# Kernel optimization log

Hardware: AMD Instinct MI355X
Metric: run time of the kernel (lower is better)

## Reference

```python
import jax, jax.numpy as jnp
import numpy as np

L, N, C = 8192, 8, 3
DIM, DIM_OUT, K, RATIO = 64, 128, 16, 0.25
L2 = int(L * RATIO)  # 2048; note L % L2 == 0 (needed for the fmod quirk)
EPS = 1e-5


def layer_norm(x, g, b):
    m = jnp.mean(x, axis=-1, keepdims=True)
    v = jnp.mean(jnp.square(x - m), axis=-1, keepdims=True)  # biased var, as torch LayerNorm
    return (x - m) * jax.lax.rsqrt(v + EPS) * g + b


def mlp(x, w1, g1, b1, w2, g2, b2):
    h = x @ w1.T
    h = layer_norm(h, g1, b1)
    h = h @ w2.T
    h = layer_norm(h, g2, b2)
    return jax.nn.relu(h)


def setup_inputs() -> dict:
    key = jax.random.key(0)
    ks = jax.random.split(key, 5)
    coords = jax.random.normal(ks[0], (L, N, C), jnp.float32)
    features = jax.random.normal(ks[1], (L, N, DIM), jnp.float32)
    s1 = 1.0 / np.sqrt(DIM)
    s2 = 1.0 / np.sqrt(DIM_OUT)
    w1 = jax.random.uniform(ks[2], (DIM_OUT, DIM), jnp.float32, -s1, s1)
    w2 = jax.random.uniform(ks[3], (DIM_OUT, DIM_OUT), jnp.float32, -s2, s2)
    g1 = jnp.ones((DIM_OUT,), jnp.float32)
    b1 = jnp.zeros((DIM_OUT,), jnp.float32)
    g2 = jnp.ones((DIM_OUT,), jnp.float32)
    b2 = jnp.zeros((DIM_OUT,), jnp.float32)
    # RandomDecimate: random permutation of point indices, keep first L2 (same across batch)
    keep_idx = jax.random.permutation(ks[4], L)[:L2].astype(jnp.int32)
    return dict(coords=coords, features=features, w1=w1, g1=g1, b1=b1,
                w2=w2, g2=g2, b2=b2, keep_idx=keep_idx)


def reference(coords, features, w1, g1, b1, w2, g2, b2, keep_idx):
    # MLP on all points: [L, N, DIM_OUT]
    feats = mlp(features, w1, g1, b1, w2, g2, b2)
    # decimation: keep_coords [L2, N, C]
    keep_coords = coords[keep_idx]
    # per-batch KNN of kept points against all points
    c = coords.transpose(1, 0, 2)        # [N, L, C]
    kc = keep_coords.transpose(1, 0, 2)  # [N, L2, C]
    d2 = (jnp.sum(kc * kc, -1)[:, :, None]
          + jnp.sum(c * c, -1)[:, None, :]
          - 2.0 * jnp.einsum('nic,njc->nij', kc, c))  # [N, L2, L]
    _, nn_idx = jax.lax.top_k(-d2, K)    # [N, L2, K] indices into [0, L)
    # faithful to clusters.fmod_(L2) on flattened idx n*L+l (L % L2 == 0 => l % L2)
    nn_idx = nn_idx % L2
    # fused gather + amax pooling over K neighbors
    fT = feats.transpose(1, 0, 2)  # [N, L, DIM_OUT]
    gathered = jax.vmap(lambda f, idx: f[idx])(fT, nn_idx)  # [N, L2, K, DIM_OUT]
    pool_features = jnp.max(gathered, axis=2).transpose(1, 0, 2)  # [L2, N, DIM_OUT]
    return keep_coords, pool_features
```

## Files before the change

### kernel.cpp

```cpp
#include <hip/hip_runtime.h>
#include <stdint.h>

#define L_    8192
#define N_    8
#define L2_   2048
#define K_    16

typedef unsigned int uint;
typedef unsigned short ushort;
typedef unsigned long long u64;
typedef __attribute__((ext_vector_type(8))) short bh8;
typedef __attribute__((ext_vector_type(4))) float f32x4;

__device__ __forceinline__ ushort f2b(float f){
  uint u = __float_as_uint(f);
  return (ushort)((u + 0x7FFFu + ((u >> 16) & 1u)) >> 16);
}
__device__ __forceinline__ uint ford(float f){
  uint u = __float_as_uint(f);
  return u ^ ((uint)((int)u >> 31) | 0x80000000u);
}
__device__ __forceinline__ float unford(uint u){
  uint v = (u & 0x80000000u) ? (u ^ 0x80000000u) : ~u;
  return __uint_as_float(v);
}

__device__ __forceinline__ void ld8(float* t, const float* p){
  float4 a = *(const float4*)p; float4 b = *(const float4*)(p + 4);
  t[0]=a.x; t[1]=a.y; t[2]=a.z; t[3]=a.w; t[4]=b.x; t[5]=b.y; t[6]=b.z; t[7]=b.w;
}
__device__ __forceinline__ bh8 pack8(const float* v){
  bh8 r;
  #pragma unroll
  for (int j = 0; j < 8; ++j) r[j] = (short)f2b(v[j]);
  return r;
}

__global__ __launch_bounds__(256) void prep_pack_k(const float* __restrict__ coords,
                                                   const int* __restrict__ keep,
                                                   const float* __restrict__ w1,
                                                   const float* __restrict__ w2,
                                                   float4* __restrict__ cF,
                                                   float* __restrict__ out0,
                                                   ushort* __restrict__ pw1,
                                                   ushort* __restrict__ pw2){
  int blk = blockIdx.x;
  int tid = threadIdx.x;
  if (blk < 96){
    int e = blk * 256 + tid;
    if (e < 8192) pw1[e] = f2b(w1[e]);
    else          pw2[e - 8192] = f2b(w2[e - 8192]);
  } else if (blk < 352){
    int e = (blk - 96) * 256 + tid;
    int l = e >> 3, n = e & 7;
    const float* cr = coords + (size_t)e * 3;
    float x = cr[0], y = cr[1], z = cr[2];
    float cc;
    {
      #pragma clang fp contract(off)
      cc = x*x + y*y + z*z;
    }
    cF[n * L_ + l] = make_float4(x, y, z, cc);
  } else {
    int t = (blk - 352) * 256 + tid;
    int i = t / 24; int rem = t - i * 24;
    out0[t] = coords[(size_t)keep[i] * 24 + rem];
  }
}

__global__ __launch_bounds__(256) void mlp_k(const float* __restrict__ feat,
                                             const ushort* __restrict__ pw1,
                                             const float* __restrict__ g1,
                                             const float* __restrict__ b1,
                                             const ushort* __restrict__ pw2,
                                             const float* __restrict__ g2,
                                             const float* __restrict__ b2,
                                             uint* __restrict__ fBw){
  __shared__ ushort hlds[64 * 136];
  int tid = threadIdx.x;
  int lane = tid & 63;
  int wv = __builtin_amdgcn_readfirstlane(tid >> 6);
  int quad = lane >> 4, c = lane & 15;
  int rowg = blockIdx.x * 64 + wv * 16;

  bh8 a1[2];
  {
    int rg = rowg + c; int l = rg & 2047, nb = rg >> 11;
    const float* xr = feat + (size_t)((l << 3) + nb) * 64 + quad * 8;
    float t[8];
    ld8(t, xr);      a1[0] = pack8(t);
    ld8(t, xr + 32); a1[1] = pack8(t);
  }

  f32x4 acc1[8];
  #pragma unroll
  for (int t = 0; t < 8; ++t) acc1[t] = (f32x4){0.f, 0.f, 0.f, 0.f};
  #pragma unroll
  for (int s = 0; s < 2; ++s){
    #pragma unroll
    for (int t = 0; t < 8; ++t){
      bh8 wb = *(const bh8*)(pw1 + (size_t)(t * 16 + c) * 64 + s * 32 + quad * 8);
      acc1[t] = __builtin_amdgcn_mfma_f32_16x16x32_bf16(a1[s], wb, acc1[t], 0, 0, 0);
    }
  }

  float mean1[4], rstd1[4];
  #pragma unroll
  for (int r = 0; r < 4; ++r){
    float s = 0.f;
    #pragma unroll
    for (int t = 0; t < 8; ++t) s += acc1[t][r];
    #pragma unroll
    for (int m = 1; m < 16; m <<= 1) s += __shfl_xor(s, m, 16);
    mean1[r] = s * 0.0078125f;
  }
  #pragma unroll
  for (int r = 0; r < 4; ++r){
    float s = 0.f;
    #pragma unroll
    for (int t = 0; t < 8; ++t){ float d = acc1[t][r] - mean1[r]; s += d * d; }
    #pragma unroll
    for (int m = 1; m < 16; m <<= 1) s += __shfl_xor(s, m, 16);
    rstd1[r] = rsqrtf(s * 0.0078125f + 1e-5f);
  }
  ushort* hl = hlds + wv * 16 * 136;
  #pragma unroll
  for (int t = 0; t < 8; ++t){
    float gv = g1[t * 16 + c], bv = b1[t * 16 + c];
    #pragma unroll
    for (int r = 0; r < 4; ++r){
      float v = (acc1[t][r] - mean1[r]) * rstd1[r] * gv + bv;
      hl[(quad * 4 + r) * 136 + t * 16 + c] = f2b(v);
    }
  }

  f32x4 acc2[8];
  #pragma unroll
  for (int t = 0; t < 8; ++t) acc2[t] = (f32x4){0.f, 0.f, 0.f, 0.f};
  #pragma unroll
  for (int s = 0; s < 4; ++s){
    bh8 af = *(const bh8*)(hl + c * 136 + s * 32 + quad * 8);
    #pragma unroll
    for (int t = 0; t < 8; ++t){
      bh8 wb = *(const bh8*)(pw2 + (size_t)(t * 16 + c) * 128 + s * 32 + quad * 8);
      acc2[t] = __builtin_amdgcn_mfma_f32_16x16x32_bf16(af, wb, acc2[t], 0, 0, 0);
    }
  }

  float mean2[4], rstd2[4];
  #pragma unroll
  for (int r = 0; r < 4; ++r){
    float s = 0.f;
    #pragma unroll
    for (int t = 0; t < 8; ++t) s += acc2[t][r];
    #pragma unroll
    for (int m = 1; m < 16; m <<= 1) s += __shfl_xor(s, m, 16);
    mean2[r] = s * 0.0078125f;
  }
  #pragma unroll
  for (int r = 0; r < 4; ++r){
    float s = 0.f;
    #pragma unroll
    for (int t = 0; t < 8; ++t){ float d = acc2[t][r] - mean2[r]; s += d * d; }
    #pragma unroll
    for (int m = 1; m < 16; m <<= 1) s += __shfl_xor(s, m, 16);
    rstd2[r] = rsqrtf(s * 0.0078125f + 1e-5f);
  }
  #pragma unroll
  for (int t = 0; t < 8; ++t){
    float gv = g2[t * 16 + c], bv = b2[t * 16 + c];
    #pragma unroll
    for (int r = 0; r < 4; ++r){
      float v = fmaxf((acc2[t][r] - mean2[r]) * rstd2[r] * gv + bv, 0.f);
      hl[(quad * 4 + r) * 136 + t * 16 + c] = f2b(v);
    }
  }

  {
    int row16 = lane >> 2, chunk = lane & 3;
    const uint* src = (const uint*)hlds + (wv * 16 + row16) * 68 + chunk * 16;
    uint* dst = fBw + (size_t)(rowg + row16) * 64 + chunk * 16;
    #pragma unroll
    for (int j = 0; j < 4; ++j)
      *(uint4*)(dst + j * 4) = *(const uint4*)(src + j * 4);
  }
}

__device__ __forceinline__ u64 shfl64(u64 v, int src){
  int lo = __shfl((int)(uint)v, src, 64);
  int hi = __shfl((int)(uint)(v >> 32), src, 64);
  return ((u64)(uint)hi << 32) | (uint)lo;
}

__device__ __forceinline__ u64 bsort64(u64 key, int lane){
  #pragma unroll
  for (int k = 2; k <= 64; k <<= 1){
    #pragma unroll
    for (int j = k >> 1; j > 0; j >>= 1){
      u64 o = shfl64(key, lane ^ j);
      bool lower = (lane & j) == 0;
      bool down  = (lane & k) == 0;
      bool takeMin = (lower == down);
      bool oLess = o < key;
      key = (oLess == takeMin) ? o : key;
    }
  }
  return key;
}
__device__ __forceinline__ u64 bmerge64(u64 key, int lane){
  #pragma unroll
  for (int j = 32; j > 0; j >>= 1){
    u64 o = shfl64(key, lane ^ j);
    bool lower = (lane & j) == 0;
    bool oLess = o < key;
    key = (oLess == lower) ? o : key;
  }
  return key;
}

__device__ __forceinline__ u64 drain(u64* ldsq, int& qcount, float& hf, int lane){
  u64 a = (lane < qcount) ? ldsq[lane] : ~0ull;
  a = bsort64(a, lane);
  if (qcount > 64){
    u64 b = (64 + lane < qcount) ? ldsq[64 + lane] : ~0ull;
    b = bsort64(b, lane);
    u64 br = shfl64(b, 63 - lane);
    a = a < br ? a : br;
    a = bmerge64(a, lane);
  }
  if (lane < 16) ldsq[lane] = a;
  u64 h = shfl64(a, 15);
  hf = unford((uint)(h >> 32));
  qcount = 16;
  return a;
}

__global__ __launch_bounds__(256) void knn_pool_k(const float4* __restrict__ cF,
                                                  const int* __restrict__ keep,
                                                  const uint* __restrict__ fB32,
                                                  float* __restrict__ out1){
  __shared__ u64 q8[4][2][128];
  int tid = threadIdx.x, lane = tid & 63;
  int wv = tid >> 6;
  int g0 = blockIdx.x * 8 + wv * 2;
  int n = g0 >> 11;
  int i0 = g0 & 2047, i1 = i0 + 1;
  u64* qlA = q8[wv][0];
  u64* qlB = q8[wv][1];
  float4 qa = cF[(n << 13) + keep[i0]];
  float4 qb = cF[(n << 13) + keep[i1]];
  const float4* base = cF + (n << 13);

  float hfA = 3.4e38f, hfrA = 3.4e38f; int qcA = 0;
  float hfB = 3.4e38f, hfrB = 3.4e38f; int qcB = 0;

  #define PROC2(cf, jidx) { \
    float dA = __builtin_fmaf(qa.x,(cf).x, __builtin_fmaf(qa.y,(cf).y, qa.z*(cf).z)); \
    float dB = __builtin_fmaf(qb.x,(cf).x, __builtin_fmaf(qb.y,(cf).y, qb.z*(cf).z)); \
    float eA = __builtin_fmaf(-2.0f, dA, qa.w + (cf).w); \
    float eB = __builtin_fmaf(-2.0f, dB, qb.w + (cf).w); \
    u64 balA = __ballot(eA <= hfrA); \
    u64 balB = __ballot(eB <= hfrB); \
    if (balA){ \
      if (eA <= hfrA){ \
        float d2; \
        { \
          _Pragma("clang fp contract(off)") \
          float dot = qa.x*(cf).x + qa.y*(cf).y + qa.z*(cf).z; \
          d2 = (qa.w + (cf).w) - 2.0f * dot; \
        } \
        int rel = __builtin_amdgcn_mbcnt_lo((uint)balA, 0); \
        rel = __builtin_amdgcn_mbcnt_hi((uint)(balA >> 32), rel); \
        qlA[qcA + rel] = ((u64)ford(d2) << 32) | (uint)(jidx); \
      } \
      qcA += __popcll(balA); \
      if (qcA >= 49){ drain(qlA, qcA, hfA, lane); hfrA = hfA + 1e-3f; } \
    } \
    if (balB){ \
      if (eB <= hfrB){ \
        float d2; \
        { \
          _Pragma("clang fp contract(off)") \
          float dot = qb.x*(cf).x + qb.y*(cf).y + qb.z*(cf).z; \
          d2 = (qb.w + (cf).w) - 2.0f * dot; \
        } \
        int rel = __builtin_amdgcn_mbcnt_lo((uint)balB, 0); \
        rel = __builtin_amdgcn_mbcnt_hi((uint)(balB >> 32), rel); \
        qlB[qcB + rel] = ((u64)ford(d2) << 32) | (uint)(jidx); \
      } \
      qcB += __popcll(balB); \
      if (qcB >= 49){ drain(qlB, qcB, hfB, lane); hfrB = hfB + 1e-3f; } \
    } \
  }

  for (int b = 0; b < 128; b += 4){
    const float4* p = base + (b << 6) + lane;
    float4 c0 = p[0];
    float4 c1 = p[64];
    float4 c2 = p[128];
    float4 c3 = p[192];
    int j0 = (b << 6) + lane;
    PROC2(c0, j0);
    PROC2(c1, j0 + 64);
    PROC2(c2, j0 + 128);
    PROC2(c3, j0 + 192);
  }
  u64 aA = drain(qlA, qcA, hfA, lane);
  u64 aB = drain(qlB, qcB, hfB, lane);
  #undef PROC2

  const uint* frow = fB32 + ((size_t)(n << 11) << 6);
  float a0 = -3.4e38f, a1v = -3.4e38f, b0 = -3.4e38f, b1v = -3.4e38f;
  #pragma unroll
  for (int k = 0; k < 16; ++k){
    int idxA = (int)(shfl64(aA, k) & 2047u);
    int idxB = (int)(shfl64(aB, k) & 2047u);
    uint uA = frow[((size_t)idxA << 6) + lane];
    uint uB = frow[((size_t)idxB << 6) + lane];
    a0  = fmaxf(a0,  __uint_as_float((uA & 0xFFFFu) << 16));
    a1v = fmaxf(a1v, __uint_as_float((uA >> 16) << 16));
    b0  = fmaxf(b0,  __uint_as_float((uB & 0xFFFFu) << 16));
    b1v = fmaxf(b1v, __uint_as_float((uB >> 16) << 16));
  }
  float2* oA = (float2*)(out1 + (size_t)(i0 * 8 + n) * 128);
  float2* oB = (float2*)(out1 + (size_t)(i1 * 8 + n) * 128);
  oA[lane] = make_float2(a0, a1v);
  oB[lane] = make_float2(b0, b1v);
}

extern "C" void kernel_launch(void* const* d_in, const int* in_sizes, int n_in,
                              void* d_out, int out_size, void* d_ws, size_t ws_size,
                              hipStream_t stream){
  const float* coords = (const float*)d_in[0];
  const float* feat   = (const float*)d_in[1];
  const float* w1     = (const float*)d_in[2];
  const float* g1     = (const float*)d_in[3];
  const float* b1     = (const float*)d_in[4];
  const float* w2     = (const float*)d_in[5];
  const float* g2     = (const float*)d_in[6];
  const float* b2     = (const float*)d_in[7];
  const int*   keep   = (const int*)d_in[8];
  float* out0 = (float*)d_out;
  float* out1 = out0 + 49152;

  char* ws = (char*)d_ws;
  float4* cF  = (float4*)ws;
  ushort* fB  = (ushort*)(ws + (1 << 20));
  ushort* pw1 = (ushort*)(ws + (5 << 20));
  ushort* pw2 = pw1 + 8192;

  hipLaunchKernelGGL(prep_pack_k, dim3(544), dim3(256), 0, stream,
                     coords, keep, w1, w2, cF, out0, pw1, pw2);
  hipLaunchKernelGGL(mlp_k, dim3(256), dim3(256), 0, stream,
                     feat, pw1, g1, b1, pw2, g2, b2, (uint*)fB);
  hipLaunchKernelGGL(knn_pool_k, dim3(2048), dim3(256), 0, stream,
                     cF, keep, (const uint*)fB, out1);
}
```

Measured before the change: 177.6 us.

## Fuse prep into MLP kernel and replace KNN drain with radix-select threshold update

Merges the weight-packing/coords-prep kernel into the MLP kernel, so each MLP block converts w1/w2 to bf16 into swizzled LDS instead of reading pre-packed global weights. This saves one launch. In the KNN kernel the distance test is rewritten as a three-FMA score against a query-shifted threshold. The full bitonic drain is replaced by a radix-select update (upd16) that finds the 16th-smallest key and compacts the candidate queue, with a larger queue and an adaptive refill trigger. The aim is fewer sort operations and less ALU work per candidate. The cost is redundant weight conversion in every MLP block and more LDS per block.

```diff
diff --git a/kernel.cpp b/kernel.cpp
--- a/kernel.cpp
+++ b/kernel.cpp
@@ -36,61 +36,72 @@
   return r;
 }
 
-__global__ __launch_bounds__(256) void prep_pack_k(const float* __restrict__ coords,
-                                                   const int* __restrict__ keep,
-                                                   const float* __restrict__ w1,
-                                                   const float* __restrict__ w2,
-                                                   float4* __restrict__ cF,
-                                                   float* __restrict__ out0,
-                                                   ushort* __restrict__ pw1,
-                                                   ushort* __restrict__ pw2){
+__global__ __launch_bounds__(256) void prep_mlp_k(const float* __restrict__ feat,
+                                                  const float* __restrict__ w1,
+                                                  const float* __restrict__ g1,
+                                                  const float* __restrict__ b1,
+                                                  const float* __restrict__ w2,
+                                                  const float* __restrict__ g2,
+                                                  const float* __restrict__ b2,
+                                                  const float* __restrict__ coords,
+                                                  const int* __restrict__ keep,
+                                                  float4* __restrict__ cF,
+                                                  float* __restrict__ out0,
+                                                  uint* __restrict__ fBw){
   int blk = blockIdx.x;
   int tid = threadIdx.x;
-  if (blk < 96){
-    int e = blk * 256 + tid;
-    if (e < 8192) pw1[e] = f2b(w1[e]);
-    else          pw2[e - 8192] = f2b(w2[e - 8192]);
-  } else if (blk < 352){
-    int e = (blk - 96) * 256 + tid;
-    int l = e >> 3, n = e & 7;
-    const float* cr = coords + (size_t)e * 3;
-    float x = cr[0], y = cr[1], z = cr[2];
-    float cc;
-    {
-      #pragma clang fp contract(off)
-      cc = x*x + y*y + z*z;
-    }
-    cF[n * L_ + l] = make_float4(x, y, z, cc);
-  } else {
-    int t = (blk - 352) * 256 + tid;
-    int i = t / 24; int rem = t - i * 24;
-    out0[t] = coords[(size_t)keep[i] * 24 + rem];
-  }
-}
-
-__global__ __launch_bounds__(256) void mlp_k(const float* __restrict__ feat,
-                                             const ushort* __restrict__ pw1,
-                                             const float* __restrict__ g1,
-                                             const float* __restrict__ b1,
-                                             const ushort* __restrict__ pw2,
-                                             const float* __restrict__ g2,
-                                             const float* __restrict__ b2,
-                                             uint* __restrict__ fBw){
-  __shared__ ushort hlds[64 * 136];
-  int tid = threadIdx.x;
+  if (blk >= 256){
+    if (blk < 512){
+      int e = (blk - 256) * 256 + tid;
+      int l = e >> 3, n = e & 7;
+      const float* cr = coords + (size_t)e * 3;
+      float x = cr[0], y = cr[1], z = cr[2];
+      float cc;
+      {
+        #pragma clang fp contract(off)
+        cc = x*x + y*y + z*z;
+      }
+      cF[n * L_ + l] = make_float4(x, y, z, cc);
+    } else {
+      int t = (blk - 512) * 256 + tid;
+      int i = t / 24; int rem = t - i * 24;
+      out0[t] = coords[(size_t)keep[i] * 24 + rem];
+    }
+    return;
+  }
+
+  __shared__ ushort w2l[128 * 128];
+  __shared__ ushort uni[64 * 136];
+  ushort* w1l  = uni;
+  ushort* hlds = uni;
+
+  for (int i = tid * 4; i < 8192; i += 1024){
+    float4 x = *(const float4*)(w1 + i);
+    int r = i >> 6, cc = i & 63;
+    ushort* d = w1l + r * 64 + (cc ^ ((r & 7) << 3));
+    d[0] = f2b(x.x); d[1] = f2b(x.y); d[2] = f2b(x.z); d[3] = f2b(x.w);
+  }
+  for (int i = tid * 4; i < 16384; i += 1024){
+    float4 x = *(const float4*)(w2 + i);
+    int r = i >> 7, cc = i & 127;
+    ushort* d = w2l + r * 128 + (cc ^ ((r & 7) << 3));
+    d[0] = f2b(x.x); d[1] = f2b(x.y); d[2] = f2b(x.z); d[3] = f2b(x.w);
+  }
+
   int lane = tid & 63;
   int wv = __builtin_amdgcn_readfirstlane(tid >> 6);
   int quad = lane >> 4, c = lane & 15;
-  int rowg = blockIdx.x * 64 + wv * 16;
+  int rowg = blk * 64 + wv * 16;
 
   bh8 a1[2];
   {
     int rg = rowg + c; int l = rg & 2047, nb = rg >> 11;
     const float* xr = feat + (size_t)((l << 3) + nb) * 64 + quad * 8;
-    float t[8];
-    ld8(t, xr);      a1[0] = pack8(t);
-    ld8(t, xr + 32); a1[1] = pack8(t);
-  }
+    float t0[8];
+    ld8(t0, xr);      a1[0] = pack8(t0);
+    ld8(t0, xr + 32); a1[1] = pack8(t0);
+  }
+  __syncthreads();
 
   f32x4 acc1[8];
   #pragma unroll
@@ -99,7 +110,7 @@
   for (int s = 0; s < 2; ++s){
     #pragma unroll
     for (int t = 0; t < 8; ++t){
-      bh8 wb = *(const bh8*)(pw1 + (size_t)(t * 16 + c) * 64 + s * 32 + quad * 8);
+      bh8 wb = *(const bh8*)(w1l + (t * 16 + c) * 64 + ((s * 32 + quad * 8) ^ ((c & 7) << 3)));
       acc1[t] = __builtin_amdgcn_mfma_f32_16x16x32_bf16(a1[s], wb, acc1[t], 0, 0, 0);
     }
   }
@@ -123,6 +134,9 @@
     for (int m = 1; m < 16; m <<= 1) s += __shfl_xor(s, m, 16);
     rstd1[r] = rsqrtf(s * 0.0078125f + 1e-5f);
   }
+
+  __syncthreads();
+
   ushort* hl = hlds + wv * 16 * 136;
   #pragma unroll
   for (int t = 0; t < 8; ++t){
@@ -142,7 +156,7 @@
     bh8 af = *(const bh8*)(hl + c * 136 + s * 32 + quad * 8);
     #pragma unroll
     for (int t = 0; t < 8; ++t){
-      bh8 wb = *(const bh8*)(pw2 + (size_t)(t * 16 + c) * 128 + s * 32 + quad * 8);
+      bh8 wb = *(const bh8*)(w2l + (t * 16 + c) * 128 + ((s * 32 + quad * 8) ^ ((c & 7) << 3)));
       acc2[t] = __builtin_amdgcn_mfma_f32_16x16x32_bf16(af, wb, acc2[t], 0, 0, 0);
     }
   }
@@ -235,11 +249,51 @@
   return a;
 }
 
+__device__ __attribute__((noinline)) u64 upd16(u64* ql, int qc, int lane){
+  uint m = 0xFFFFFFFFu;
+  #pragma clang loop unroll(disable)
+  for (int s = lane; s < qc; s += 64){
+    uint h = (uint)(ql[s] >> 32);
+    m = (h < m) ? h : m;
+  }
+  uint v = 0u;
+  #pragma clang loop unroll(disable)
+  for (int b = 31; b >= 0; --b){
+    uint tv = v | (1u << b);
+    if (__popcll(__ballot(m < tv)) < 16) v = tv;
+  }
+  int out = 0;
+  #pragma clang loop unroll(disable)
+  for (int s0 = 0; s0 < qc; s0 += 64){
+    int s = s0 + lane;
+    u64 k = (s < qc) ? ql[s] : ~0ull;
+    bool kp = (s < qc) && ((uint)(k >> 32) <= v);
+    u64 bal = __ballot(kp);
+    int rel = __builtin_amdgcn_mbcnt_lo((uint)bal, 0);
+    rel = __builtin_amdgcn_mbcnt_hi((uint)(bal >> 32), rel);
+    if (kp) ql[out + rel] = k;
+    out += __popcll(bal);
+  }
+  while (out > 128){
+    int qt = 128; float dm;
+    drain(ql, qt, dm, lane);
+    int mv = out - 128;
+    #pragma clang loop unroll(disable)
+    for (int s0 = 0; s0 < mv; s0 += 64){
+      int s = s0 + lane;
+      u64 k = (s < mv) ? ql[128 + s] : 0ull;
+      if (s < mv) ql[16 + s] = k;
+    }
+    out = 16 + mv;
+  }
+  return ((u64)v << 32) | (uint)out;
+}
+
 __global__ __launch_bounds__(256) void knn_pool_k(const float4* __restrict__ cF,
                                                   const int* __restrict__ keep,
                                                   const uint* __restrict__ fB32,
                                                   float* __restrict__ out1){
-  __shared__ u64 q8[4][2][128];
+  __shared__ u64 q8[4][2][256];
   int tid = threadIdx.x, lane = tid & 63;
   int wv = tid >> 6;
   int g0 = blockIdx.x * 8 + wv * 2;
@@ -251,18 +305,18 @@
   float4 qb = cF[(n << 13) + keep[i1]];
   const float4* base = cF + (n << 13);
 
-  float hfA = 3.4e38f, hfrA = 3.4e38f; int qcA = 0;
-  float hfB = 3.4e38f, hfrB = 3.4e38f; int qcB = 0;
+  float q2ax = -2.f * qa.x, q2ay = -2.f * qa.y, q2az = -2.f * qa.z;
+  float q2bx = -2.f * qb.x, q2by = -2.f * qb.y, q2bz = -2.f * qb.z;
+  float tA = 3.4e38f, tB = 3.4e38f;
+  int qcA = 0, qcB = 0, nxA = 64, nxB = 64;
 
   #define PROC2(cf, jidx) { \
-    float dA = __builtin_fmaf(qa.x,(cf).x, __builtin_fmaf(qa.y,(cf).y, qa.z*(cf).z)); \
-    float dB = __builtin_fmaf(qb.x,(cf).x, __builtin_fmaf(qb.y,(cf).y, qb.z*(cf).z)); \
-    float eA = __builtin_fmaf(-2.0f, dA, qa.w + (cf).w); \
-    float eB = __builtin_fmaf(-2.0f, dB, qb.w + (cf).w); \
-    u64 balA = __ballot(eA <= hfrA); \
-    u64 balB = __ballot(eB <= hfrB); \
+    float sA = __builtin_fmaf(q2ax,(cf).x, __builtin_fmaf(q2ay,(cf).y, __builtin_fmaf(q2az,(cf).z,(cf).w))); \
+    float sB = __builtin_fmaf(q2bx,(cf).x, __builtin_fmaf(q2by,(cf).y, __builtin_fmaf(q2bz,(cf).z,(cf).w))); \
+    u64 balA = __ballot(sA <= tA); \
+    u64 balB = __ballot(sB <= tB); \
     if (balA){ \
-      if (eA <= hfrA){ \
+      if (sA <= tA){ \
         float d2; \
         { \
           _Pragma("clang fp contract(off)") \
@@ -274,10 +328,13 @@
         qlA[qcA + rel] = ((u64)ford(d2) << 32) | (uint)(jidx); \
       } \
       qcA += __popcll(balA); \
-      if (qcA >= 49){ drain(qlA, qcA, hfA, lane); hfrA = hfA + 1e-3f; } \
+      if (qcA >= nxA){ \
+        u64 ru = upd16(qlA, qcA, lane); qcA = (int)(ru & 0xFFFFFFFFu); \
+        tA = unford((uint)(ru >> 32)) + 1e-3f - qa.w; nxA = qcA + 48; \
+      } \
     } \
     if (balB){ \
-      if (eB <= hfrB){ \
+      if (sB <= tB){ \
         float d2; \
         { \
           _Pragma("clang fp contract(off)") \
@@ -289,7 +346,10 @@
         qlB[qcB + rel] = ((u64)ford(d2) << 32) | (uint)(jidx); \
       } \
       qcB += __popcll(balB); \
-      if (qcB >= 49){ drain(qlB, qcB, hfB, lane); hfrB = hfB + 1e-3f; } \
+      if (qcB >= nxB){ \
+        u64 ru = upd16(qlB, qcB, lane); qcB = (int)(ru & 0xFFFFFFFFu); \
+        tB = unford((uint)(ru >> 32)) + 1e-3f - qb.w; nxB = qcB + 48; \
+      } \
     } \
   }
 
@@ -305,9 +365,17 @@
     PROC2(c2, j0 + 128);
     PROC2(c3, j0 + 192);
   }
-  u64 aA = drain(qlA, qcA, hfA, lane);
-  u64 aB = drain(qlB, qcB, hfB, lane);
   #undef PROC2
+
+  {
+    u64 ru = upd16(qlA, qcA, lane); qcA = (int)(ru & 0xFFFFFFFFu);
+  }
+  {
+    u64 ru = upd16(qlB, qcB, lane); qcB = (int)(ru & 0xFFFFFFFFu);
+  }
+  float dmy;
+  u64 aA = drain(qlA, qcA, dmy, lane);
+  u64 aB = drain(qlB, qcB, dmy, lane);
 
   const uint* frow = fB32 + ((size_t)(n << 11) << 6);
   float a0 = -3.4e38f, a1v = -3.4e38f, b0 = -3.4e38f, b1v = -3.4e38f;
@@ -346,13 +414,9 @@
   char* ws = (char*)d_ws;
   float4* cF  = (float4*)ws;
   ushort* fB  = (ushort*)(ws + (1 << 20));
-  ushort* pw1 = (ushort*)(ws + (5 << 20));
-  ushort* pw2 = pw1 + 8192;
-
-  hipLaunchKernelGGL(prep_pack_k, dim3(544), dim3(256), 0, stream,
-                     coords, keep, w1, w2, cF, out0, pw1, pw2);
-  hipLaunchKernelGGL(mlp_k, dim3(256), dim3(256), 0, stream,
-                     feat, pw1, g1, b1, pw2, g2, b2, (uint*)fB);
+
+  hipLaunchKernelGGL(prep_mlp_k, dim3(704), dim3(256), 0, stream,
+                     feat, w1, g1, b1, w2, g2, b2, coords, keep, cF, out0, (uint*)fB);
   hipLaunchKernelGGL(knn_pool_k, dim3(2048), dim3(256), 0, stream,
                      cF, keep, (const uint*)fB, out1);
 }
```

Measured after the change: 189.3 us. 1.07x slower.

## Replace full queue sort with radix-select threshold compaction in KNN candidate filtering

Applied to the files above, without the earlier changes.

The per-wave candidate queue is no longer fully bitonic-sorted each time it fills. Instead a 16-bit radix select over the high key bits finds an approximate 16th-smallest threshold, and survivors are compacted with ballot/mbcnt. The full sort runs only when more than 64 survive, and the sort routine is made noinline to cut code size. The distance filter is also rewritten to fold -2q and the query-norm offset into three FMAs per candidate. In exchange the threshold is looser, so more candidates may pass and the queue may refill more often.

```diff
diff --git a/kernel.cpp b/kernel.cpp
--- a/kernel.cpp
+++ b/kernel.cpp
@@ -218,7 +218,7 @@
   return key;
 }
 
-__device__ __forceinline__ u64 drain(u64* ldsq, int& qcount, float& hf, int lane){
+__device__ __attribute__((noinline)) u64 drainx(u64* ldsq, int qcount, int lane){
   u64 a = (lane < qcount) ? ldsq[lane] : ~0ull;
   a = bsort64(a, lane);
   if (qcount > 64){
@@ -229,10 +229,46 @@
     a = bmerge64(a, lane);
   }
   if (lane < 16) ldsq[lane] = a;
-  u64 h = shfl64(a, 15);
-  hf = unford((uint)(h >> 32));
-  qcount = 16;
   return a;
+}
+
+__device__ __forceinline__ void updq(u64* ql, int& qc, int& nx, float& thr,
+                                     float qw, int lane){
+  int q = qc;
+  u64 k0 = (lane < q) ? ql[lane] : ~0ull;
+  u64 k1 = (64 + lane < q) ? ql[64 + lane] : ~0ull;
+  uint h0 = (uint)(k0 >> 32), h1 = (uint)(k1 >> 32);
+  uint m = h0 < h1 ? h0 : h1;
+  uint v = 0u;
+  #pragma unroll
+  for (int b = 31; b >= 16; --b){
+    uint tv = v | (1u << b);
+    if (__popcll(__ballot(m < tv)) < 16) v = tv;
+  }
+  uint vb = (v >= 0xFFFF0000u) ? 0xFFFFFFFFu : (v + 0x10000u);
+
+  bool kp0 = (h0 <= vb);
+  u64 bal0 = __ballot(kp0);
+  int r0 = __builtin_amdgcn_mbcnt_lo((uint)bal0, 0);
+  r0 = __builtin_amdgcn_mbcnt_hi((uint)(bal0 >> 32), r0);
+  if (kp0) ql[r0] = k0;
+  int c0 = __popcll(bal0);
+  bool kp1 = (h1 <= vb);
+  u64 bal1 = __ballot(kp1);
+  int r1 = __builtin_amdgcn_mbcnt_lo((uint)bal1, 0);
+  r1 = __builtin_amdgcn_mbcnt_hi((uint)(bal1 >> 32), r1);
+  if (kp1) ql[c0 + r1] = k1;
+  int out = c0 + __popcll(bal1);
+
+  uint hb = vb;
+  if (out > 64){
+    u64 a = drainx(ql, out, lane);
+    hb = (uint)(shfl64(a, 15) >> 32);
+    out = 16;
+  }
+  qc = out;
+  nx = out + 33;
+  thr = unford(hb) + 1e-3f - qw;
 }
 
 __global__ __launch_bounds__(256) void knn_pool_k(const float4* __restrict__ cF,
@@ -251,18 +287,18 @@
   float4 qb = cF[(n << 13) + keep[i1]];
   const float4* base = cF + (n << 13);
 
-  float hfA = 3.4e38f, hfrA = 3.4e38f; int qcA = 0;
-  float hfB = 3.4e38f, hfrB = 3.4e38f; int qcB = 0;
+  float q2ax = -2.f * qa.x, q2ay = -2.f * qa.y, q2az = -2.f * qa.z;
+  float q2bx = -2.f * qb.x, q2by = -2.f * qb.y, q2bz = -2.f * qb.z;
+  float tA = 3.4e38f, tB = 3.4e38f;
+  int qcA = 0, qcB = 0, nxA = 49, nxB = 49;
 
   #define PROC2(cf, jidx) { \
-    float dA = __builtin_fmaf(qa.x,(cf).x, __builtin_fmaf(qa.y,(cf).y, qa.z*(cf).z)); \
-    float dB = __builtin_fmaf(qb.x,(cf).x, __builtin_fmaf(qb.y,(cf).y, qb.z*(cf).z)); \
-    float eA = __builtin_fmaf(-2.0f, dA, qa.w + (cf).w); \
-    float eB = __builtin_fmaf(-2.0f, dB, qb.w + (cf).w); \
-    u64 balA = __ballot(eA <= hfrA); \
-    u64 balB = __ballot(eB <= hfrB); \
+    float sA = __builtin_fmaf(q2ax,(cf).x, __builtin_fmaf(q2ay,(cf).y, __builtin_fmaf(q2az,(cf).z,(cf).w))); \
+    float sB = __builtin_fmaf(q2bx,(cf).x, __builtin_fmaf(q2by,(cf).y, __builtin_fmaf(q2bz,(cf).z,(cf).w))); \
+    u64 balA = __ballot(sA <= tA); \
+    u64 balB = __ballot(sB <= tB); \
     if (balA){ \
-      if (eA <= hfrA){ \
+      if (sA <= tA){ \
         float d2; \
         { \
           _Pragma("clang fp contract(off)") \
@@ -274,10 +310,10 @@
         qlA[qcA + rel] = ((u64)ford(d2) << 32) | (uint)(jidx); \
       } \
       qcA += __popcll(balA); \
-      if (qcA >= 49){ drain(qlA, qcA, hfA, lane); hfrA = hfA + 1e-3f; } \
+      if (qcA >= nxA) updq(qlA, qcA, nxA, tA, qa.w, lane); \
     } \
     if (balB){ \
-      if (eB <= hfrB){ \
+      if (sB <= tB){ \
         float d2; \
         { \
           _Pragma("clang fp contract(off)") \
@@ -289,7 +325,7 @@
         qlB[qcB + rel] = ((u64)ford(d2) << 32) | (uint)(jidx); \
       } \
       qcB += __popcll(balB); \
-      if (qcB >= 49){ drain(qlB, qcB, hfB, lane); hfrB = hfB + 1e-3f; } \
+      if (qcB >= nxB) updq(qlB, qcB, nxB, tB, qb.w, lane); \
     } \
   }
 
@@ -305,9 +341,10 @@
     PROC2(c2, j0 + 128);
     PROC2(c3, j0 + 192);
   }
-  u64 aA = drain(qlA, qcA, hfA, lane);
-  u64 aB = drain(qlB, qcB, hfB, lane);
   #undef PROC2
+
+  u64 aA = drainx(qlA, qcA, lane);
+  u64 aB = drainx(qlB, qcB, lane);
 
   const uint* frow = fB32 + ((size_t)(n << 11) << 6);
   float a0 = -3.4e38f, a1v = -3.4e38f, b0 = -3.4e38f, b1v = -3.4e38f;
```

After: 161.2 us. 1.1x faster.
